# Kernel tuning notes

Measured on AMD Instinct MI355X. Metric: run time of the kernel, lower is better.

The kernel has to match this reference:

```python
import jax, jax.numpy as jnp
import numpy as np

HIDDEN = 768  # hidden_dim of the embedding matrix
VOCAB = 30522


def setup_inputs() -> dict:
    key = jax.random.key(0)
    k1, k2, k3, k4, k5, k6 = jax.random.split(key, 6)
    core = jax.random.normal(k1, (40, 256, 256), dtype=jnp.float32)
    f0 = jax.random.normal(k2, (40, 40), dtype=jnp.float32)
    f1 = jax.random.normal(k3, (768, 256), dtype=jnp.float32)
    f2 = jax.random.normal(k4, (768, 256), dtype=jnp.float32)
    ids = jax.random.randint(k5, (8192,), 0, VOCAB, dtype=jnp.int32)
    x = jax.random.normal(k6, (8192, 768), dtype=jnp.float32)  # unused by forward, kept for signature parity
    return {"x": x, "ids": ids, "core": core, "f0": f0, "f1": f1, "f2": f2}


def reference(x, ids, core, f0, f1, f2):
    # tucker_to_tensor: core x_0 f0 x_1 f1 x_2 f2 -> (40, 768, 768)
    res = jnp.einsum('abc,ia,jb,kc->ijk', core, f0, f1, f2)
    # flatten to padded embedding table (30720, 768) and gather requested rows
    table = res.reshape(-1, HIDDEN)
    return table[ids, :]
```

## Files before the change

### kernel.cpp

```cpp
#include <hip/hip_runtime.h>


#define A_DIM 40
#define BC 65536
#define C_DIM 256
#define HID 768
#define CAP 320

typedef __attribute__((ext_vector_type(8))) short short8;
typedef __attribute__((ext_vector_type(4))) float floatx4;

#define AS1 __attribute__((address_space(1)))
#define AS3 __attribute__((address_space(3)))

__device__ __forceinline__ void gl2lds16(const unsigned short* g, unsigned short* l) {
    __builtin_amdgcn_global_load_lds((const AS1 unsigned int*)g, (AS3 unsigned int*)l,
                                     16, 0, 0);
}

__device__ __forceinline__ unsigned short f2bf(float f) {
    unsigned int u = __builtin_bit_cast(unsigned int, f);
    u += 0x7FFFu + ((u >> 16) & 1u);
    return (unsigned short)(u >> 16);
}

__global__ __launch_bounds__(256) void k01_fused(const float* __restrict__ core,
                                                 const float* __restrict__ f0,
                                                 const float* __restrict__ f1,
                                                 const float* __restrict__ f2,
                                                 const int* __restrict__ ids,
                                                 unsigned short* __restrict__ A1t,
                                                 unsigned short* __restrict__ f1b,
                                                 unsigned short* __restrict__ f2b,
                                                 int* __restrict__ jslot,
                                                 int* __restrict__ tilecnt) {
    const int bid = blockIdx.x;
    const int tid = threadIdx.x;
    if (bid < 512) {
        __shared__ float f0s[200];
        __shared__ unsigned short tt[32 * 34];
        const int i0 = (bid >> 6) * 5;
        const int tile = bid & 63;
        const int b0 = (tile >> 3) * 32;
        const int c0 = (tile & 7) * 32;
        if (tid < 200) f0s[tid] = f0[i0 * A_DIM + tid];
        __syncthreads();

        const int pb = (tid >> 4) * 2;
        const int pc = (tid & 15) * 2;
        float acc[5][4];
#pragma unroll
        for (int ii = 0; ii < 5; ++ii)
#pragma unroll
            for (int e = 0; e < 4; ++e) acc[ii][e] = 0.f;

        const float* cp0 = core + (b0 + pb) * 256 + (c0 + pc);
        for (int a = 0; a < A_DIM; ++a) {
            const float* cp = cp0 + a * BC;
            const float2 r0 = *(const float2*)cp;
            const float2 r1 = *(const float2*)(cp + 256);
#pragma unroll
            for (int ii = 0; ii < 5; ++ii) {
                const float fa = f0s[ii * A_DIM + a];
                acc[ii][0] += fa * r0.x;
                acc[ii][1] += fa * r0.y;
                acc[ii][2] += fa * r1.x;
                acc[ii][3] += fa * r1.y;
            }
        }
        const int rc = tid >> 3;
        const int rb4 = (tid & 7) * 4;
#pragma unroll
        for (int ii = 0; ii < 5; ++ii) {
            if (ii) __syncthreads();
            unsigned short e00 = f2bf(acc[ii][0]);
            unsigned short e10 = f2bf(acc[ii][2]);
            unsigned short e01 = f2bf(acc[ii][1]);
            unsigned short e11 = f2bf(acc[ii][3]);
            *(unsigned int*)&tt[pc * 34 + pb]       = (unsigned int)e00 | ((unsigned int)e10 << 16);
            *(unsigned int*)&tt[(pc + 1) * 34 + pb] = (unsigned int)e01 | ((unsigned int)e11 << 16);
            __syncthreads();
            unsigned short o[4];
#pragma unroll
            for (int u = 0; u < 4; ++u) o[u] = tt[rc * 34 + rb4 + u];
            unsigned int lo = (unsigned int)o[0] | ((unsigned int)o[1] << 16);
            unsigned int hi = (unsigned int)o[2] | ((unsigned int)o[3] << 16);
            *(uint2*)&A1t[(size_t)(i0 + ii) * BC + (c0 + rc) * 256 + b0 + rb4] = make_uint2(lo, hi);
        }
    } else if (bid < 896) {
        const int idx = (bid - 512) * 256 + tid;
        const float* src;
        unsigned short* dst;
        int off;
        if (idx < 49152) { src = f1; dst = f1b; off = idx; }
        else             { src = f2; dst = f2b; off = idx - 49152; }
        const float4 v = *(const float4*)&src[off * 4];
        const unsigned int lo = (unsigned int)f2bf(v.x) | ((unsigned int)f2bf(v.y) << 16);
        const unsigned int hi = (unsigned int)f2bf(v.z) | ((unsigned int)f2bf(v.w) << 16);
        *(uint2*)&dst[off * 4] = make_uint2(lo, hi);
    } else {
        const int i = bid - 896;
        __shared__ int cnt;
        if (tid == 0) cnt = 0;
        __syncthreads();
        const unsigned int lo_id = (unsigned int)i * 768u;
        for (int t = tid; t < 8192; t += 256) {
            const unsigned int id = (unsigned int)ids[t];
            const unsigned int d = id - lo_id;
            if (d < 768u) {
                const int s = atomicAdd(&cnt, 1);
                jslot[i * CAP + s] = (int)d;
            }
        }
        __syncthreads();
        const int u = cnt;
        const int tc = (u + 63) >> 6;
        if (tid == 0) tilecnt[i] = tc;
        for (int s = u + tid; s < tc * 64; s += 256) jslot[i * CAP + s] = 0;
    }
}

__global__ __launch_bounds__(256) void k2_gemm(const unsigned short* __restrict__ f1b,
                                               const unsigned short* __restrict__ A1t,
                                               const int* __restrict__ jslot,
                                               const int* __restrict__ tilecnt,
                                               unsigned short* __restrict__ A2) {
    const int T = blockIdx.y;
    const int i = T / 5, t = T % 5;
    if (t >= tilecnt[i]) return;
    const int c0 = blockIdx.x * 64;
    const int slot0 = i * CAP + t * 64;
    const unsigned short* __restrict__ Bsrc = A1t + i * BC;

    __shared__ int js[64];
    __shared__ unsigned short As[64 * 32];
    __shared__ unsigned short Bs[64 * 32];

    const int tid = threadIdx.x;
    if (tid < 64) js[tid] = jslot[slot0 + tid];
    __syncthreads();

    const int lane = tid & 63, wave = tid >> 6;
    const int wm = (wave >> 1) * 32, wn = (wave & 1) * 32;
    const int l16 = lane & 15, q = lane >> 4;

    const int r0 = tid >> 2, o0 = (tid & 3) * 8;
    const size_t ga = (size_t)js[r0] * 256;
    unsigned short* AsW = &As[wave * 512];
    unsigned short* BsW = &Bs[wave * 512];

    floatx4 acc[2][2];
#pragma unroll
    for (int p = 0; p < 2; ++p)
#pragma unroll
        for (int r = 0; r < 2; ++r) acc[p][r] = (floatx4)0.f;

    for (int kk = 0; kk < C_DIM; kk += 32) {
        gl2lds16(&f1b[ga + kk + o0], AsW);
        gl2lds16(&Bsrc[(c0 + r0) * 256 + kk + o0], BsW);
        __syncthreads();
        short8 af[2], bf[2];
#pragma unroll
        for (int p = 0; p < 2; ++p) af[p] = *(const short8*)&As[(wm + p * 16 + l16) * 32 + q * 8];
#pragma unroll
        for (int r = 0; r < 2; ++r) bf[r] = *(const short8*)&Bs[(wn + r * 16 + l16) * 32 + q * 8];
#pragma unroll
        for (int p = 0; p < 2; ++p)
#pragma unroll
            for (int r = 0; r < 2; ++r)
                acc[p][r] = __builtin_amdgcn_mfma_f32_16x16x32_bf16(af[p], bf[r], acc[p][r], 0, 0, 0);
        __syncthreads();
    }
#pragma unroll
    for (int p = 0; p < 2; ++p)
#pragma unroll
        for (int r = 0; r < 2; ++r)
#pragma unroll
            for (int rr = 0; rr < 4; ++rr) {
                const int jrow = js[wm + p * 16 + q * 4 + rr];
                const int col = c0 + wn + r * 16 + l16;
                A2[(size_t)(i * HID + jrow) * 256 + col] = f2bf(acc[p][r][rr]);
            }
}

__global__ __launch_bounds__(256) void k3_gemm(const unsigned short* __restrict__ A2,
                                               const unsigned short* __restrict__ f2b,
                                               const int* __restrict__ ids,
                                               float* __restrict__ out) {
    const int n0 = blockIdx.x * 64;
    const int k0 = blockIdx.y * 64;

    __shared__ int ids_s[64];
    __shared__ unsigned short As[64 * 32];
    __shared__ unsigned short Bs[64 * 32];

    const int tid = threadIdx.x;
    if (tid < 64) ids_s[tid] = ids[n0 + tid];
    __syncthreads();

    const int lane = tid & 63, wave = tid >> 6;
    const int wm = (wave >> 1) * 32, wn = (wave & 1) * 32;
    const int l16 = lane & 15, q = lane >> 4;

    const int r0 = tid >> 2, o0 = (tid & 3) * 8;
    const size_t ga = (size_t)ids_s[r0] * 256;
    unsigned short* AsW = &As[wave * 512];
    unsigned short* BsW = &Bs[wave * 512];

    floatx4 acc[2][2];
#pragma unroll
    for (int p = 0; p < 2; ++p)
#pragma unroll
        for (int r = 0; r < 2; ++r) acc[p][r] = (floatx4)0.f;

    for (int kk = 0; kk < C_DIM; kk += 32) {
        gl2lds16(&A2[ga + kk + o0], AsW);
        gl2lds16(&f2b[(k0 + r0) * 256 + kk + o0], BsW);
        __syncthreads();
        short8 af[2], bf[2];
#pragma unroll
        for (int p = 0; p < 2; ++p) af[p] = *(const short8*)&As[(wm + p * 16 + l16) * 32 + q * 8];
#pragma unroll
        for (int r = 0; r < 2; ++r) bf[r] = *(const short8*)&Bs[(wn + r * 16 + l16) * 32 + q * 8];
#pragma unroll
        for (int p = 0; p < 2; ++p)
#pragma unroll
            for (int r = 0; r < 2; ++r)
                acc[p][r] = __builtin_amdgcn_mfma_f32_16x16x32_bf16(af[p], bf[r], acc[p][r], 0, 0, 0);
        __syncthreads();
    }
#pragma unroll
    for (int p = 0; p < 2; ++p)
#pragma unroll
        for (int r = 0; r < 2; ++r)
#pragma unroll
            for (int rr = 0; rr < 4; ++rr) {
                const int row = n0 + wm + p * 16 + q * 4 + rr;
                const int col = k0 + wn + r * 16 + l16;
                out[(size_t)row * HID + col] = acc[p][r][rr];
            }
}

extern "C" void kernel_launch(void* const* d_in, const int* in_sizes, int n_in,
                              void* d_out, int out_size, void* d_ws, size_t ws_size,
                              hipStream_t stream) {
    const int*   ids  = (const int*)d_in[1];
    const float* core = (const float*)d_in[2];
    const float* f0   = (const float*)d_in[3];
    const float* f1   = (const float*)d_in[4];
    const float* f2   = (const float*)d_in[5];
    float* out = (float*)d_out;

    char* ws = (char*)d_ws;
    unsigned short* A1t   = (unsigned short*)ws;
    unsigned short* A2    = (unsigned short*)(ws + 5242880);
    unsigned short* f1b   = (unsigned short*)(ws + 20971520);
    unsigned short* f2b   = (unsigned short*)(ws + 21364736);
    int*            jslot = (int*)(ws + 21757952);
    int*            tcnt  = (int*)(ws + 21809152);

    k01_fused<<<936, 256, 0, stream>>>(core, f0, f1, f2, ids, A1t, f1b, f2b, jslot, tcnt);
    k2_gemm<<<dim3(4, 200), 256, 0, stream>>>(f1b, A1t, jslot, tcnt, A2);
    k3_gemm<<<dim3(128, 12), 256, 0, stream>>>(A2, f2b, ids, out);
}
```

Before: 114.7 us.

## Read core once per block in mode-0 stage and widen k3 GEMM tile to 128 columns

The first stage is restructured so each of 256 blocks loads a 16x16 (b,c) patch of core for all 40 a-values into registers once. It then produces all 40 output i-slices, reading f0 directly from global memory instead of re-reading core for each group of 5 i values. The final gather-GEMM tile grows from 64x64 to 64x128, so each A2 row fetch is reused across twice as many output columns and the grid is halved. The costs are higher register pressure (40-float arrays plus 8 accumulator tiles), fewer blocks in stage one, and narrower 2-byte A1t stores.

```diff
diff --git a/kernel.cpp b/kernel.cpp
--- a/kernel.cpp
+++ b/kernel.cpp
@@ -36,59 +36,38 @@
                                                  int* __restrict__ tilecnt) {
     const int bid = blockIdx.x;
     const int tid = threadIdx.x;
-    if (bid < 512) {
-        __shared__ float f0s[200];
-        __shared__ unsigned short tt[32 * 34];
-        const int i0 = (bid >> 6) * 5;
-        const int tile = bid & 63;
-        const int b0 = (tile >> 3) * 32;
-        const int c0 = (tile & 7) * 32;
-        if (tid < 200) f0s[tid] = f0[i0 * A_DIM + tid];
-        __syncthreads();
-
-        const int pb = (tid >> 4) * 2;
-        const int pc = (tid & 15) * 2;
-        float acc[5][4];
-#pragma unroll
-        for (int ii = 0; ii < 5; ++ii)
-#pragma unroll
-            for (int e = 0; e < 4; ++e) acc[ii][e] = 0.f;
-
-        const float* cp0 = core + (b0 + pb) * 256 + (c0 + pc);
-        for (int a = 0; a < A_DIM; ++a) {
-            const float* cp = cp0 + a * BC;
-            const float2 r0 = *(const float2*)cp;
-            const float2 r1 = *(const float2*)(cp + 256);
-#pragma unroll
-            for (int ii = 0; ii < 5; ++ii) {
-                const float fa = f0s[ii * A_DIM + a];
-                acc[ii][0] += fa * r0.x;
-                acc[ii][1] += fa * r0.y;
-                acc[ii][2] += fa * r1.x;
-                acc[ii][3] += fa * r1.y;
-            }
+    if (bid < 256) {
+        const int b0 = (bid >> 4) * 16;
+        const int c0 = (bid & 15) * 16;
+        const int lb = tid >> 4, lc = tid & 15;
+        float cv[A_DIM];
+        const float* cp = core + (b0 + lb) * 256 + (c0 + lc);
+#pragma unroll
+        for (int a = 0; a < A_DIM; ++a) cv[a] = cp[a * BC];
+
+        __shared__ unsigned short tt[8][16 * 17];
+        const int wlc = tid >> 4, wlb = tid & 15;
+        for (int i0 = 0; i0 < A_DIM; i0 += 8) {
+            unsigned short res[8];
+#pragma unroll
+            for (int ii = 0; ii < 8; ++ii) {
+                float s = 0.f;
+                const float* f0r = f0 + (i0 + ii) * A_DIM;
+#pragma unroll
+                for (int a = 0; a < A_DIM; ++a) s += f0r[a] * cv[a];
+                res[ii] = f2bf(s);
+            }
+            __syncthreads();
+#pragma unroll
+            for (int ii = 0; ii < 8; ++ii) tt[ii][lc * 17 + lb] = res[ii];
+            __syncthreads();
+#pragma unroll
+            for (int ii = 0; ii < 8; ++ii)
+                A1t[(size_t)(i0 + ii) * BC + (c0 + wlc) * 256 + b0 + wlb] =
+                    tt[ii][wlc * 17 + wlb];
         }
-        const int rc = tid >> 3;
-        const int rb4 = (tid & 7) * 4;
-#pragma unroll
-        for (int ii = 0; ii < 5; ++ii) {
-            if (ii) __syncthreads();
-            unsigned short e00 = f2bf(acc[ii][0]);
-            unsigned short e10 = f2bf(acc[ii][2]);
-            unsigned short e01 = f2bf(acc[ii][1]);
-            unsigned short e11 = f2bf(acc[ii][3]);
-            *(unsigned int*)&tt[pc * 34 + pb]       = (unsigned int)e00 | ((unsigned int)e10 << 16);
-            *(unsigned int*)&tt[(pc + 1) * 34 + pb] = (unsigned int)e01 | ((unsigned int)e11 << 16);
-            __syncthreads();
-            unsigned short o[4];
-#pragma unroll
-            for (int u = 0; u < 4; ++u) o[u] = tt[rc * 34 + rb4 + u];
-            unsigned int lo = (unsigned int)o[0] | ((unsigned int)o[1] << 16);
-            unsigned int hi = (unsigned int)o[2] | ((unsigned int)o[3] << 16);
-            *(uint2*)&A1t[(size_t)(i0 + ii) * BC + (c0 + rc) * 256 + b0 + rb4] = make_uint2(lo, hi);
-        }
-    } else if (bid < 896) {
-        const int idx = (bid - 512) * 256 + tid;
+    } else if (bid < 640) {
+        const int idx = (bid - 256) * 256 + tid;
         const float* src;
         unsigned short* dst;
         int off;
@@ -99,7 +78,7 @@
         const unsigned int hi = (unsigned int)f2bf(v.z) | ((unsigned int)f2bf(v.w) << 16);
         *(uint2*)&dst[off * 4] = make_uint2(lo, hi);
     } else {
-        const int i = bid - 896;
+        const int i = bid - 640;
         __shared__ int cnt;
         if (tid == 0) cnt = 0;
         __syncthreads();
@@ -188,55 +167,58 @@
                                                const int* __restrict__ ids,
                                                float* __restrict__ out) {
     const int n0 = blockIdx.x * 64;
-    const int k0 = blockIdx.y * 64;
+    const int k0 = blockIdx.y * 128;
 
     __shared__ int ids_s[64];
     __shared__ unsigned short As[64 * 32];
-    __shared__ unsigned short Bs[64 * 32];
+    __shared__ unsigned short Bs[128 * 32];
 
     const int tid = threadIdx.x;
     if (tid < 64) ids_s[tid] = ids[n0 + tid];
     __syncthreads();
 
     const int lane = tid & 63, wave = tid >> 6;
-    const int wm = (wave >> 1) * 32, wn = (wave & 1) * 32;
+    const int wm = (wave & 1) * 32;
+    const int wk = (wave >> 1) * 64;
     const int l16 = lane & 15, q = lane >> 4;
 
     const int r0 = tid >> 2, o0 = (tid & 3) * 8;
     const size_t ga = (size_t)ids_s[r0] * 256;
-    unsigned short* AsW = &As[wave * 512];
-    unsigned short* BsW = &Bs[wave * 512];
-
-    floatx4 acc[2][2];
-#pragma unroll
-    for (int p = 0; p < 2; ++p)
-#pragma unroll
-        for (int r = 0; r < 2; ++r) acc[p][r] = (floatx4)0.f;
+    unsigned short* AsW  = &As[wave * 512];
+    unsigned short* BsW0 = &Bs[wave * 512];
+    unsigned short* BsW1 = &Bs[2048 + wave * 512];
+
+    floatx4 acc[2][4];
+#pragma unroll
+    for (int p = 0; p < 2; ++p)
+#pragma unroll
+        for (int r = 0; r < 4; ++r) acc[p][r] = (floatx4)0.f;
 
     for (int kk = 0; kk < C_DIM; kk += 32) {
         gl2lds16(&A2[ga + kk + o0], AsW);
-        gl2lds16(&f2b[(k0 + r0) * 256 + kk + o0], BsW);
-        __syncthreads();
-        short8 af[2], bf[2];
+        gl2lds16(&f2b[(k0 + r0) * 256 + kk + o0], BsW0);
+        gl2lds16(&f2b[(k0 + 64 + r0) * 256 + kk + o0], BsW1);
+        __syncthreads();
+        short8 af[2], bf[4];
 #pragma unroll
         for (int p = 0; p < 2; ++p) af[p] = *(const short8*)&As[(wm + p * 16 + l16) * 32 + q * 8];
 #pragma unroll
-        for (int r = 0; r < 2; ++r) bf[r] = *(const short8*)&Bs[(wn + r * 16 + l16) * 32 + q * 8];
+        for (int r = 0; r < 4; ++r) bf[r] = *(const short8*)&Bs[(wk + r * 16 + l16) * 32 + q * 8];
 #pragma unroll
         for (int p = 0; p < 2; ++p)
 #pragma unroll
-            for (int r = 0; r < 2; ++r)
+            for (int r = 0; r < 4; ++r)
                 acc[p][r] = __builtin_amdgcn_mfma_f32_16x16x32_bf16(af[p], bf[r], acc[p][r], 0, 0, 0);
         __syncthreads();
     }
 #pragma unroll
     for (int p = 0; p < 2; ++p)
 #pragma unroll
-        for (int r = 0; r < 2; ++r)
+        for (int r = 0; r < 4; ++r)
 #pragma unroll
             for (int rr = 0; rr < 4; ++rr) {
                 const int row = n0 + wm + p * 16 + q * 4 + rr;
-                const int col = k0 + wn + r * 16 + l16;
+                const int col = k0 + wk + r * 16 + l16;
                 out[(size_t)row * HID + col] = acc[p][r][rr];
             }
 }
@@ -259,7 +241,7 @@
     int*            jslot = (int*)(ws + 21757952);
     int*            tcnt  = (int*)(ws + 21809152);
 
-    k01_fused<<<936, 256, 0, stream>>>(core, f0, f1, f2, ids, A1t, f1b, f2b, jslot, tcnt);
+    k01_fused<<<680, 256, 0, stream>>>(core, f0, f1, f2, ids, A1t, f1b, f2b, jslot, tcnt);
     k2_gemm<<<dim3(4, 200), 256, 0, stream>>>(f1b, A1t, jslot, tcnt, A2);
-    k3_gemm<<<dim3(128, 12), 256, 0, stream>>>(A2, f2b, ids, out);
-}
+    k3_gemm<<<dim3(128, 6), 256, 0, stream>>>(A2, f2b, ids, out);
+}
```

New measurement: 127.8 us. +11.4%, slower.
